# Kernel optimization log

Measured on AMD Instinct MI355X. Metric: run time of the kernel, lower is better.

The kernel has to match this reference:

```python
import jax, jax.numpy as jnp
import numpy as np
from jax import lax

V, E, HD, T = 32000, 256, 256, 4   # vocab, embed dim, lstm hidden (bidir total), tagset (BMES)
H = HD // 2                        # hidden per direction
B, S = 64, 1024


def setup_inputs() -> dict:
    key = jax.random.key(0)
    ks = jax.random.split(key, 16)
    sc = 0.1
    return {
        "sentences": jax.random.randint(ks[0], (B, S), 0, V, dtype=jnp.int32),
        "embed": jax.random.normal(ks[1], (V, E), jnp.float32) * sc,
        "w_ih_f": jax.random.normal(ks[2], (4 * H, E), jnp.float32) * sc,
        "w_hh_f": jax.random.normal(ks[3], (4 * H, H), jnp.float32) * sc,
        "b_ih_f": jax.random.normal(ks[4], (4 * H,), jnp.float32) * sc,
        "b_hh_f": jax.random.normal(ks[5], (4 * H,), jnp.float32) * sc,
        "w_ih_r": jax.random.normal(ks[6], (4 * H, E), jnp.float32) * sc,
        "w_hh_r": jax.random.normal(ks[7], (4 * H, H), jnp.float32) * sc,
        "b_ih_r": jax.random.normal(ks[8], (4 * H,), jnp.float32) * sc,
        "b_hh_r": jax.random.normal(ks[9], (4 * H,), jnp.float32) * sc,
        "w_out": jax.random.normal(ks[10], (T, HD), jnp.float32) * sc,
        "b_out": jax.random.normal(ks[11], (T,), jnp.float32) * sc,
        "start_t": jax.random.normal(ks[12], (T,), jnp.float32) * sc,
        "end_t": jax.random.normal(ks[13], (T,), jnp.float32) * sc,
        "trans": jax.random.normal(ks[14], (T, T), jnp.float32) * sc,
    }


def _lstm_pass(x, w_ih, w_hh, b_ih, b_hh):
    # x: [S, B, E]; PyTorch gate order i, f, g, o; zero initial state.
    bsz = x.shape[1]
    hdim = w_hh.shape[1]
    b = b_ih + b_hh

    def step(carry, xt):
        h, c = carry
        z = xt @ w_ih.T + h @ w_hh.T + b  # [B, 4H]
        i, f, g, o = jnp.split(z, 4, axis=-1)
        c = jax.nn.sigmoid(f) * c + jax.nn.sigmoid(i) * jnp.tanh(g)
        h = jax.nn.sigmoid(o) * jnp.tanh(c)
        return (h, c), h

    init = (jnp.zeros((bsz, hdim), x.dtype), jnp.zeros((bsz, hdim), x.dtype))
    _, hs = lax.scan(step, init, x)
    return hs  # [S, B, H]


def _emissions(sentences, embed, w_ih_f, w_hh_f, b_ih_f, b_hh_f,
               w_ih_r, w_hh_r, b_ih_r, b_hh_r, w_out, b_out):
    x = embed[sentences]                # [B, S, E]
    xs = jnp.transpose(x, (1, 0, 2))    # [S, B, E]
    hf = _lstm_pass(xs, w_ih_f, w_hh_f, b_ih_f, b_hh_f)
    hr = _lstm_pass(xs[::-1], w_ih_r, w_hh_r, b_ih_r, b_hh_r)[::-1]
    h = jnp.concatenate([hf, hr], axis=-1)        # [S, B, 2H]
    return h @ w_out.T + b_out                    # [S, B, T] emissions


def _viterbi_decode(feats, start_t, end_t, trans):
    # feats: [S, B, T] (no mask: all sequences full length, matching crf.decode on dense batch)
    score0 = start_t + feats[0]  # [B, T]

    def fwd_step(score, emit):
        nxt = score[:, :, None] + trans[None, :, :] + emit[:, None, :]  # [B, Tprev, Tcur]
        return jnp.max(nxt, axis=1), jnp.argmax(nxt, axis=1)

    final, bps = lax.scan(fwd_step, score0, feats[1:])  # bps: [S-1, B, T]
    final = final + end_t
    last = jnp.argmax(final, axis=1)  # [B]

    def back_step(tag, bp):
        prev = jnp.take_along_axis(bp, tag[:, None], axis=1)[:, 0]
        return prev, prev

    _, path_head = lax.scan(back_step, last, bps, reverse=True)  # [S-1, B], tags at t=0..S-2
    path = jnp.concatenate([path_head, last[None]], axis=0)      # [S, B]
    return jnp.transpose(path, (1, 0)).astype(jnp.int32)         # [B, S]


def reference(sentences, embed, w_ih_f, w_hh_f, b_ih_f, b_hh_f,
              w_ih_r, w_hh_r, b_ih_r, b_hh_r, w_out, b_out,
              start_t, end_t, trans):
    feats = _emissions(sentences, embed, w_ih_f, w_hh_f, b_ih_f, b_hh_f,
                       w_ih_r, w_hh_r, b_ih_r, b_hh_r, w_out, b_out)
    return _viterbi_decode(feats, start_t, end_t, trans)
```

## Files before the change

### kernel.cpp

```cpp
#include <hip/hip_runtime.h>
#include <cstdint>
#include <cstddef>

#define SLEN 1024
#define BATCH 64
#define EDIM 256
#define HDIM 128
#define GDIM 512
#define NTAG 4

typedef float f2 __attribute__((ext_vector_type(2)));
typedef float f4 __attribute__((ext_vector_type(4)));


__device__ __forceinline__ float sigm_f(float x) {
    return 1.0f / (1.0f + __expf(-x));
}
__device__ __forceinline__ float tanh_f(float x) {
    return 1.0f - 2.0f / (1.0f + __expf(2.0f * x));
}

template <int CTRL>
__device__ __forceinline__ float quad_perm(float x) {
    return __int_as_float(
        __builtin_amdgcn_mov_dpp(__float_as_int(x), CTRL, 0xF, 0xF, true));
}
#define QP_XOR1 0xB1
#define QP_XOR2 0x4E
#define QP_MIR8 0x141
#define QP_BC0  0x00
#define QP_BC1  0x55
#define QP_BC2  0xAA
#define QP_BC3  0xFF

__device__ __forceinline__ void gemm_body(
    float* smem, int mt, int cp,
    const int* __restrict__ sent, const float* __restrict__ embed,
    const float* __restrict__ w_ih_f, const float* __restrict__ w_ih_r,
    const float* __restrict__ b_ih_f, const float* __restrict__ b_hh_f,
    const float* __restrict__ b_ih_r, const float* __restrict__ b_hh_r,
    float* __restrict__ Z, int base_f, int base_r)
{
    float* As = smem;
    const int t  = threadIdx.x;
    const int tm = t >> 8;
    const int tt = t & 255;
    float* Bs = smem + 4096 + tm * 4096;

    const int nt  = cp * 2 + tm;
    const int dir = nt >> 2;
    const float* W  = dir ? w_ih_r : w_ih_f;
    const float* bi = dir ? b_ih_r : b_ih_f;
    const float* bh = dir ? b_hh_r : b_hh_f;
    const int ncol = (nt & 3) * 128;
    const int r0   = mt * 128;

    const int sra = t & 127;
    const int qa  = t >> 7;
    const int r_loc = r0 + sra;
    const int s_loc = r_loc >> 6;
    const int b_    = r_loc & 63;
    const int s_glob = (dir ? base_r : base_f) + s_loc;
    const int tok = sent[b_ * SLEN + s_glob];
    const float* arow = embed + (size_t)tok * EDIM + qa * 8;

    const int srb = tt & 127;
    const int hb  = tt >> 7;
    const float* brow = W + (size_t)(ncol + srb) * EDIM + hb * 16;

    const int tx = tt & 15, ty = tt >> 4;

    f2 acc[8][4];
    #pragma unroll
    for (int i = 0; i < 8; ++i)
        #pragma unroll
        for (int jj = 0; jj < 4; ++jj) acc[i][jj] = (f2)(0.0f);

    for (int kt = 0; kt < 8; ++kt) {
        const int k0 = kt * 32;
        __syncthreads();
        {
            float4 v0 = *(const float4*)(arow + k0);
            float4 v1 = *(const float4*)(arow + k0 + 4);
            const int kk = qa * 8;
            As[(kk + 0) * 128 + sra] = v0.x;
            As[(kk + 1) * 128 + sra] = v0.y;
            As[(kk + 2) * 128 + sra] = v0.z;
            As[(kk + 3) * 128 + sra] = v0.w;
            As[(kk + 4) * 128 + sra] = v1.x;
            As[(kk + 5) * 128 + sra] = v1.y;
            As[(kk + 6) * 128 + sra] = v1.z;
            As[(kk + 7) * 128 + sra] = v1.w;
        }
        #pragma unroll
        for (int i = 0; i < 4; ++i) {
            float4 v = *(const float4*)(brow + k0 + i * 4);
            const int kk = hb * 16 + i * 4;
            Bs[(kk + 0) * 128 + srb] = v.x;
            Bs[(kk + 1) * 128 + srb] = v.y;
            Bs[(kk + 2) * 128 + srb] = v.z;
            Bs[(kk + 3) * 128 + srb] = v.w;
        }
        __syncthreads();

        #pragma unroll 8
        for (int k = 0; k < 32; ++k) {
            const f4 a0  = *(const f4*)&As[k * 128 + ty * 4];
            const f4 a1  = *(const f4*)&As[k * 128 + 64 + ty * 4];
            const f4 bq0 = *(const f4*)&Bs[k * 128 + tx * 4];
            const f4 bq1 = *(const f4*)&Bs[k * 128 + 64 + tx * 4];
            float av[8] = {a0.x, a0.y, a0.z, a0.w, a1.x, a1.y, a1.z, a1.w};
            f2 bv[4];
            bv[0] = __builtin_shufflevector(bq0, bq0, 0, 1);
            bv[1] = __builtin_shufflevector(bq0, bq0, 2, 3);
            bv[2] = __builtin_shufflevector(bq1, bq1, 0, 1);
            bv[3] = __builtin_shufflevector(bq1, bq1, 2, 3);
            #pragma unroll
            for (int i = 0; i < 8; ++i) {
                f2 as; as.x = av[i]; as.y = av[i];
                #pragma unroll
                for (int jj = 0; jj < 4; ++jj)
                    acc[i][jj] += as * bv[jj];
            }
        }
    }

    float bias0[4], bias1[4];
    #pragma unroll
    for (int j = 0; j < 4; ++j) {
        bias0[j] = bi[ncol + tx * 4 + j] + bh[ncol + tx * 4 + j];
        bias1[j] = bi[ncol + 64 + tx * 4 + j] + bh[ncol + 64 + tx * 4 + j];
    }

    #pragma unroll
    for (int i = 0; i < 8; ++i) {
        const int row = r0 + ((i < 4) ? (ty * 4 + i) : (64 + ty * 4 + i - 4));
        float* zp = Z + (size_t)row * 1024 + dir * 512 + ncol;
        float4 o0, o1;
        o0.x = acc[i][0].x + bias0[0]; o0.y = acc[i][0].y + bias0[1];
        o0.z = acc[i][1].x + bias0[2]; o0.w = acc[i][1].y + bias0[3];
        o1.x = acc[i][2].x + bias1[0]; o1.y = acc[i][2].y + bias1[1];
        o1.z = acc[i][3].x + bias1[2]; o1.w = acc[i][3].y + bias1[3];
        *(float4*)(zp + tx * 4)      = o0;
        *(float4*)(zp + 64 + tx * 4) = o1;
    }
}

__device__ __forceinline__ void lstm_body(
    float* smem,
    const float* __restrict__ Z, const float* __restrict__ w_hh_f,
    const float* __restrict__ w_hh_r, float* __restrict__ H,
    float* __restrict__ ST, int base_f, int base_r, int L, int first)
{
    float* sh_h = smem;

    const int bid = blockIdx.x;
    const int b   = bid & 63;
    const int dir = bid >> 6;
    const int q   = threadIdx.x;
    const int p   = q & 7;
    const int Q   = q >> 3;
    const int gt  = p & 3;
    const int hi  = p >> 2;
    const int u   = Q + hi * 64;

    const float* Whh = dir ? w_hh_r : w_hh_f;

    f2 w2[8][8];
    #pragma unroll
    for (int pr = 0; pr < 8; ++pr) {
        const int uu = (pr & 4) ? (Q + 64) : Q;
        const int gg = pr & 3;
        const f2* src =
            (const f2*)(Whh + ((size_t)(gg * 128 + uu) * 128 + p * 16));
        #pragma unroll
        for (int i = 0; i < 8; ++i) w2[pr][i] = src[i];
    }

    float* stp = ST + (size_t)(dir * 64 + b) * 256;
    if (q < 128)
        sh_h[(q >> 5) * 36 + (q & 31)] = first ? 0.0f : stp[q];
    float c = first ? 0.0f : stp[128 + u];

    const ptrdiff_t zstride = dir ? -65536 : 65536;
    const float* zp0 = Z + (size_t)b * 1024 + dir * 512
                     + (dir ? (size_t)(L - 1) * 65536 : 0) + gt * 128 + u;
    const ptrdiff_t hstride = dir ? -16384 : 16384;
    float* hg = H + ((size_t)(dir ? (base_r + L - 1) : base_f) * 64 + b) * 256
              + dir * 128 + u;

    const bool k4 = (p & 4) != 0;
    const bool k2 = (p & 2) != 0;
    const bool k1 = (p & 1) != 0;
    const float gsc  = (gt == 2) ? 2.0f : 1.0f;
    const float gofs = (gt == 2) ? -1.0f : 0.0f;
    const int shr = (p >> 1) * 36 + (p & 1) * 16;
    const int shw = (u >> 5) * 36 + (u & 31);

    float zcur[4], znxt[4];
    {
        const float* zp = zp0;
        #pragma unroll
        for (int dt = 0; dt < 4; ++dt) { zcur[dt] = *zp; zp += zstride; }
    }
    __syncthreads();

    float hlast = 0.0f;

    for (int t0 = 0; t0 < L; t0 += 4) {
        const bool more = (t0 + 4 < L);
        if (more) {
            const float* zp = zp0 + (ptrdiff_t)(t0 + 4) * zstride;
            #pragma unroll
            for (int dt = 0; dt < 4; ++dt) { znxt[dt] = *zp; zp += zstride; }
        }

        #pragma unroll
        for (int dt = 0; dt < 4; ++dt) {
            const f4* hp = (const f4*)(sh_h + (dt & 1) * 160 + shr);
            f2 hv[8];
            #pragma unroll
            for (int i = 0; i < 4; ++i) {
                f4 v = hp[i];
                hv[2 * i]     = __builtin_shufflevector(v, v, 0, 1);
                hv[2 * i + 1] = __builtin_shufflevector(v, v, 2, 3);
            }
            float s[8];
            #pragma unroll
            for (int pr = 0; pr < 8; ++pr) {
                f2 a = (f2)(0.0f);
                #pragma unroll
                for (int i = 0; i < 8; ++i) a += w2[pr][i] * hv[i];
                s[pr] = a.x + a.y;
            }
            float K1[4];
            #pragma unroll
            for (int j = 0; j < 4; ++j) {
                float keep = k4 ? s[j + 4] : s[j];
                float send = k4 ? s[j] : s[j + 4];
                K1[j] = keep + quad_perm<QP_MIR8>(send);
            }
            float K2[2];
            #pragma unroll
            for (int j = 0; j < 2; ++j) {
                float keep = k2 ? K1[j + 2] : K1[j];
                float send = k2 ? K1[j] : K1[j + 2];
                K2[j] = keep + quad_perm<QP_XOR2>(send);
            }
            float keep3 = k1 ? K2[1] : K2[0];
            float send3 = k1 ? K2[0] : K2[1];
            float zv = keep3 + quad_perm<QP_XOR1>(send3) + zcur[dt];

            float sgv = sigm_f(zv * gsc);
            float act = fmaf(sgv, gsc, gofs);

            float a_i = quad_perm<QP_BC0>(act);
            float a_f = quad_perm<QP_BC1>(act);
            float a_g = quad_perm<QP_BC2>(act);
            float a_o = quad_perm<QP_BC3>(act);
            c = a_f * c + a_i * a_g;
            float h = a_o * tanh_f(c);
            hlast = h;

            if (gt == 0) {
                sh_h[((dt + 1) & 1) * 160 + shw] = h;
                *hg = h;
            }
            hg += hstride;
            __syncthreads();
        }

        if (more) {
            #pragma unroll
            for (int dt = 0; dt < 4; ++dt) zcur[dt] = znxt[dt];
        }
    }

    if (gt == 0) {
        stp[u] = hlast;
        stp[128 + u] = c;
    }
}

__global__ __launch_bounds__(512) void fused_lstm_gemm(
    const int* __restrict__ sent, const float* __restrict__ embed,
    const float* __restrict__ w_ih_f, const float* __restrict__ w_ih_r,
    const float* __restrict__ b_ih_f, const float* __restrict__ b_hh_f,
    const float* __restrict__ b_ih_r, const float* __restrict__ b_hh_r,
    float* __restrict__ Zw, int gbase_f, int gbase_r, int mtiles,
    const float* __restrict__ Zr, const float* __restrict__ w_hh_f,
    const float* __restrict__ w_hh_r, float* __restrict__ H,
    float* __restrict__ ST, int lbase_f, int lbase_r, int L, int first)
{
    __shared__ __align__(16) float smem[12288];

    if (blockIdx.x < 128) {
        lstm_body(smem, Zr, w_hh_f, w_hh_r, H, ST, lbase_f, lbase_r, L, first);
    } else {
        const int g  = blockIdx.x - 128;
        const int mt = g % mtiles;
        const int cp = g / mtiles;
        gemm_body(smem, mt, cp, sent, embed, w_ih_f, w_ih_r,
                  b_ih_f, b_hh_f, b_ih_r, b_hh_r, Zw, gbase_f, gbase_r);
    }
}

__global__ __launch_bounds__(512) void gemm_zin(
    const int* __restrict__ sent, const float* __restrict__ embed,
    const float* __restrict__ w_ih_f, const float* __restrict__ w_ih_r,
    const float* __restrict__ b_ih_f, const float* __restrict__ b_hh_f,
    const float* __restrict__ b_ih_r, const float* __restrict__ b_hh_r,
    float* __restrict__ Z, int base_f, int base_r)
{
    __shared__ __align__(16) float smem[12288];
    gemm_body(smem, blockIdx.x, blockIdx.y, sent, embed, w_ih_f, w_ih_r,
              b_ih_f, b_hh_f, b_ih_r, b_hh_r, Z, base_f, base_r);
}

__global__ __launch_bounds__(256) void emissions_k(
    const float* __restrict__ H, const float* __restrict__ w_out,
    const float* __restrict__ b_out, float* __restrict__ F)
{
    const int gid = blockIdx.x * 256 + threadIdx.x;
    const int r   = gid >> 2;
    const int tg  = gid & 3;
    const float4* h4 = (const float4*)(H + (size_t)r * 256);
    const float4* w4 = (const float4*)(w_out + (size_t)tg * 256);
    float a0 = 0.f, a1 = 0.f, a2 = 0.f, a3 = 0.f;
    #pragma unroll 8
    for (int k = 0; k < 64; ++k) {
        float4 h = h4[k], w = w4[k];
        a0 = fmaf(h.x, w.x, a0); a1 = fmaf(h.y, w.y, a1);
        a2 = fmaf(h.z, w.z, a2); a3 = fmaf(h.w, w.w, a3);
    }
    F[gid] = ((a0 + a1) + (a2 + a3)) + b_out[tg];
}

__device__ __forceinline__ unsigned compose_map(unsigned a, unsigned b) {
    unsigned r = 0;
    #pragma unroll
    for (int jj = 0; jj < 4; ++jj) {
        unsigned bj = (b >> (jj * 8)) & 3u;
        unsigned aj = (a >> (bj * 8)) & 3u;
        r |= aj << (jj * 8);
    }
    return r;
}

__global__ __launch_bounds__(64) void viterbi_k(
    const float* __restrict__ F, const float* __restrict__ start_t,
    const float* __restrict__ end_t, const float* __restrict__ trans,
    int* __restrict__ out)
{
    const int b    = blockIdx.x;
    const int lane = threadIdx.x;
    __shared__ __align__(16) float sfeat[SLEN][NTAG];
    __shared__ unsigned sbp[SLEN];

    #pragma unroll
    for (int i = 0; i < 16; ++i) {
        int s = i * 64 + lane;
        ((float4*)sfeat)[s] = *(const float4*)(F + ((size_t)s * BATCH + b) * NTAG);
    }
    __syncthreads();

    const int cur = lane & 3;
    float tr0 = trans[0 * 4 + cur], tr1 = trans[1 * 4 + cur];
    float tr2 = trans[2 * 4 + cur], tr3 = trans[3 * 4 + cur];
    float sc = start_t[cur] + sfeat[0][cur];

    for (int s = 1; s < SLEN; ++s) {
        float ft = sfeat[s][cur];
        float s0 = __shfl(sc, 0), s1 = __shfl(sc, 1);
        float s2 = __shfl(sc, 2), s3 = __shfl(sc, 3);
        float c0 = s0 + tr0, c1 = s1 + tr1, c2 = s2 + tr2, c3 = s3 + tr3;
        float best = c0; int arg = 0;
        if (c1 > best) { best = c1; arg = 1; }
        if (c2 > best) { best = c2; arg = 2; }
        if (c3 > best) { best = c3; arg = 3; }
        sc = best + ft;
        unsigned bp = (unsigned)arg;
        unsigned b0 = __shfl(bp, 0), b1 = __shfl(bp, 1);
        unsigned b2 = __shfl(bp, 2), b3 = __shfl(bp, 3);
        if (lane == 0) sbp[s] = b0 | (b1 << 8) | (b2 << 16) | (b3 << 24);
    }
    sc += end_t[cur];
    float f0 = __shfl(sc, 0), f1 = __shfl(sc, 1);
    float f2v = __shfl(sc, 2), f3 = __shfl(sc, 3);
    int last = 0; float bb = f0;
    if (f1 > bb)  { bb = f1;  last = 1; }
    if (f2v > bb) { bb = f2v; last = 2; }
    if (f3 > bb)  { bb = f3;  last = 3; }
    __syncthreads();

    unsigned m[16];
    #pragma unroll
    for (int k = 0; k < 16; ++k) {
        int s = lane * 16 + k;
        m[k] = (s >= 1) ? sbp[s] : 0x03020100u;
    }
    unsigned G = m[15];
    #pragma unroll
    for (int k = 14; k >= 0; --k) G = compose_map(m[k], G);
    unsigned R = G;
    #pragma unroll
    for (int d = 1; d < 64; d <<= 1) {
        unsigned oo = __shfl_down(R, d);
        if (lane + d < 64) R = compose_map(R, oo);
    }
    unsigned P = __shfl_down(R, 1);
    if (lane == 63) P = 0x03020100u;

    int tcur = (int)((P >> (last * 8)) & 3u);
    int* ob = out + b * SLEN + lane * 16;
    ob[15] = tcur;
    #pragma unroll
    for (int k = 15; k >= 1; --k) {
        tcur = (int)((m[k] >> (tcur * 8)) & 3u);
        ob[k - 1] = tcur;
    }
}

extern "C" void kernel_launch(void* const* d_in, const int* in_sizes, int n_in,
                              void* d_out, int out_size, void* d_ws, size_t ws_size,
                              hipStream_t stream)
{
    const int*   sent    = (const int*)d_in[0];
    const float* embed   = (const float*)d_in[1];
    const float* w_ih_f  = (const float*)d_in[2];
    const float* w_hh_f  = (const float*)d_in[3];
    const float* b_ih_f  = (const float*)d_in[4];
    const float* b_hh_f  = (const float*)d_in[5];
    const float* w_ih_r  = (const float*)d_in[6];
    const float* w_hh_r  = (const float*)d_in[7];
    const float* b_ih_r  = (const float*)d_in[8];
    const float* b_hh_r  = (const float*)d_in[9];
    const float* w_out   = (const float*)d_in[10];
    const float* b_out   = (const float*)d_in[11];
    const float* start_t = (const float*)d_in[12];
    const float* end_t   = (const float*)d_in[13];
    const float* trans   = (const float*)d_in[14];
    int* out = (int*)d_out;

    const size_t H_FLOATS  = (size_t)SLEN * BATCH * 256;
    const size_t F_FLOATS  = (size_t)SLEN * BATCH * NTAG;
    const size_t ST_FLOATS = (size_t)2 * BATCH * 256;
    const size_t FIXED = H_FLOATS + F_FLOATS + ST_FLOATS;

    int L = 0;
    for (int cand = 256; cand >= 32; cand >>= 1) {
        size_t need = ((size_t)2 * cand * BATCH * 1024 + FIXED) * sizeof(float);
        if (need <= ws_size) { L = cand; break; }
    }

    if (L > 0) {
        const int nch = SLEN / L;
        const int mtiles = (L * BATCH) / 128;
        float* Z0 = (float*)d_ws;
        float* Z1 = Z0 + (size_t)L * BATCH * 1024;
        float* H  = Z1 + (size_t)L * BATCH * 1024;
        float* F  = H + H_FLOATS;
        float* ST = F + F_FLOATS;
        float* Zb[2] = {Z0, Z1};

        gemm_zin<<<dim3(mtiles, 4), 512, 0, stream>>>(
            sent, embed, w_ih_f, w_ih_r, b_ih_f, b_hh_f, b_ih_r, b_hh_r,
            Zb[0], 0, SLEN - L);

        for (int c = 0; c < nch; ++c) {
            const int lbase_f = c * L;
            const int lbase_r = SLEN - (c + 1) * L;
            const int hasg = (c + 1 < nch);
            const int gbase_f = (c + 1) * L;
            const int gbase_r = SLEN - (c + 2) * L;
            const int grid = hasg ? (128 + mtiles * 4) : 128;
            fused_lstm_gemm<<<grid, 512, 0, stream>>>(
                sent, embed, w_ih_f, w_ih_r, b_ih_f, b_hh_f, b_ih_r, b_hh_r,
                Zb[(c + 1) & 1], hasg ? gbase_f : 0, hasg ? gbase_r : 0, mtiles,
                Zb[c & 1], w_hh_f, w_hh_r, H, ST, lbase_f, lbase_r, L,
                c == 0 ? 1 : 0);
        }

        emissions_k<<<1024, 256, 0, stream>>>(H, w_out, b_out, F);
        viterbi_k<<<64, 64, 0, stream>>>(F, start_t, end_t, trans, out);
    } else {
        int Ls = SLEN;
        while (Ls > 32) {
            size_t need = ((size_t)Ls * BATCH * 1024 + FIXED) * sizeof(float);
            if (need <= ws_size) break;
            Ls >>= 1;
        }
        const int nch = SLEN / Ls;
        const int mtiles = (Ls * BATCH) / 128;
        float* Z  = (float*)d_ws;
        float* H  = Z + (size_t)Ls * BATCH * 1024;
        float* F  = H + H_FLOATS;
        float* ST = F + F_FLOATS;

        for (int c = 0; c < nch; ++c) {
            const int base_f = c * Ls;
            const int base_r = SLEN - (c + 1) * Ls;
            gemm_zin<<<dim3(mtiles, 4), 512, 0, stream>>>(
                sent, embed, w_ih_f, w_ih_r, b_ih_f, b_hh_f, b_ih_r, b_hh_r,
                Z, base_f, base_r);
            fused_lstm_gemm<<<128, 512, 0, stream>>>(
                sent, embed, w_ih_f, w_ih_r, b_ih_f, b_hh_f, b_ih_r, b_hh_r,
                Z, 0, 0, mtiles,
                Z, w_hh_f, w_hh_r, H, ST, base_f, base_r, Ls, c == 0 ? 1 : 0);
        }
        emissions_k<<<1024, 256, 0, stream>>>(H, w_out, b_out, F);
        viterbi_k<<<64, 64, 0, stream>>>(F, start_t, end_t, trans, out);
    }
}
```

Measured before the change: 1.182 ms.

## Process two batch rows per LSTM block, streaming recurrent weights from memory

Restructures the recurrent LSTM kernel so each block advances two batch sequences at once, halving the number of LSTM blocks. Each thread now owns one hidden unit and a quarter of K for all four gates. Recurrent weights are read from global memory each step instead of being kept in registers. The intent is to amortise weight traffic across two sequences and free CUs for the overlapped input GEMM. The risk is longer per-step latency on the serial recurrence from cache-bound weight loads.

```diff
diff --git a/kernel.cpp b/kernel.cpp
--- a/kernel.cpp
+++ b/kernel.cpp
@@ -27,11 +27,12 @@
 }
 #define QP_XOR1 0xB1
 #define QP_XOR2 0x4E
-#define QP_MIR8 0x141
 #define QP_BC0  0x00
 #define QP_BC1  0x55
 #define QP_BC2  0xAA
 #define QP_BC3  0xFF
+
+#define HPAD(k) ((k) + (((k) >> 5) << 2))
 
 __device__ __forceinline__ void gemm_body(
     float* smem, int mt, int cp,
@@ -155,116 +156,141 @@
     float* sh_h = smem;
 
     const int bid = blockIdx.x;
-    const int b   = bid & 63;
-    const int dir = bid >> 6;
+    const int dir = bid >> 5;
+    const int b0  = (bid & 31) * 2;
     const int q   = threadIdx.x;
-    const int p   = q & 7;
-    const int Q   = q >> 3;
-    const int gt  = p & 3;
-    const int hi  = p >> 2;
-    const int u   = Q + hi * 64;
+    const int u   = q >> 2;
+    const int p   = q & 3;
 
     const float* Whh = dir ? w_hh_r : w_hh_f;
-
-    f2 w2[8][8];
-    #pragma unroll
-    for (int pr = 0; pr < 8; ++pr) {
-        const int uu = (pr & 4) ? (Q + 64) : Q;
-        const int gg = pr & 3;
-        const f2* src =
-            (const f2*)(Whh + ((size_t)(gg * 128 + uu) * 128 + p * 16));
-        #pragma unroll
-        for (int i = 0; i < 8; ++i) w2[pr][i] = src[i];
-    }
-
-    float* stp = ST + (size_t)(dir * 64 + b) * 256;
-    if (q < 128)
-        sh_h[(q >> 5) * 36 + (q & 31)] = first ? 0.0f : stp[q];
-    float c = first ? 0.0f : stp[128 + u];
+    const float* wbase = Whh + (size_t)u * 128 + p * 32;
+
+    float* stp0 = ST + (size_t)(dir * 64 + b0) * 256;
+
+    if (q < 256) {
+        const int bb = q >> 7, uu = q & 127;
+        sh_h[bb * 144 + HPAD(uu)] =
+            first ? 0.0f : ST[(size_t)(dir * 64 + b0 + bb) * 256 + uu];
+    }
+    float c0 = first ? 0.0f : stp0[128 + u];
+    float c1 = first ? 0.0f : stp0[256 + 128 + u];
 
     const ptrdiff_t zstride = dir ? -65536 : 65536;
-    const float* zp0 = Z + (size_t)b * 1024 + dir * 512
-                     + (dir ? (size_t)(L - 1) * 65536 : 0) + gt * 128 + u;
+    const float* zp0 = Z + (size_t)b0 * 1024 + dir * 512 + p * 128 + u
+                     + (dir ? (size_t)(L - 1) * 65536 : 0);
     const ptrdiff_t hstride = dir ? -16384 : 16384;
-    float* hg = H + ((size_t)(dir ? (base_r + L - 1) : base_f) * 64 + b) * 256
+    float* hg = H + ((size_t)(dir ? (base_r + L - 1) : base_f) * 64 + b0) * 256
               + dir * 128 + u;
 
-    const bool k4 = (p & 4) != 0;
     const bool k2 = (p & 2) != 0;
     const bool k1 = (p & 1) != 0;
-    const float gsc  = (gt == 2) ? 2.0f : 1.0f;
-    const float gofs = (gt == 2) ? -1.0f : 0.0f;
-    const int shr = (p >> 1) * 36 + (p & 1) * 16;
-    const int shw = (u >> 5) * 36 + (u & 31);
-
-    float zcur[4], znxt[4];
+    const float gsc  = (p == 2) ? 2.0f : 1.0f;
+    const float gofs = (p == 2) ? -1.0f : 0.0f;
+    const int rbase = 36 * p;
+
+    float zc[4][2], zn[4][2];
     {
         const float* zp = zp0;
         #pragma unroll
-        for (int dt = 0; dt < 4; ++dt) { zcur[dt] = *zp; zp += zstride; }
+        for (int dt = 0; dt < 4; ++dt) {
+            zc[dt][0] = zp[0]; zc[dt][1] = zp[1024]; zp += zstride;
+        }
     }
     __syncthreads();
 
-    float hlast = 0.0f;
+    float h0l = 0.0f, h1l = 0.0f;
 
     for (int t0 = 0; t0 < L; t0 += 4) {
         const bool more = (t0 + 4 < L);
         if (more) {
             const float* zp = zp0 + (ptrdiff_t)(t0 + 4) * zstride;
             #pragma unroll
-            for (int dt = 0; dt < 4; ++dt) { znxt[dt] = *zp; zp += zstride; }
+            for (int dt = 0; dt < 4; ++dt) {
+                zn[dt][0] = zp[0]; zn[dt][1] = zp[1024]; zp += zstride;
+            }
         }
 
         #pragma unroll
         for (int dt = 0; dt < 4; ++dt) {
-            const f4* hp = (const f4*)(sh_h + (dt & 1) * 160 + shr);
-            f2 hv[8];
-            #pragma unroll
-            for (int i = 0; i < 4; ++i) {
-                f4 v = hp[i];
-                hv[2 * i]     = __builtin_shufflevector(v, v, 0, 1);
-                hv[2 * i + 1] = __builtin_shufflevector(v, v, 2, 3);
-            }
-            float s[8];
-            #pragma unroll
-            for (int pr = 0; pr < 8; ++pr) {
-                f2 a = (f2)(0.0f);
+            float* shb = sh_h + ((t0 + dt) & 1) * 288;
+            f2 acc[4][2];
+            #pragma unroll
+            for (int g = 0; g < 4; ++g) {
+                acc[g][0] = (f2)(0.0f); acc[g][1] = (f2)(0.0f);
+            }
+
+            #pragma unroll
+            for (int kh = 0; kh < 2; ++kh) {
+                const f4* h0p = (const f4*)(shb + rbase + kh * 16);
+                const f4* h1p = (const f4*)(shb + 144 + rbase + kh * 16);
+                f2 ha[8], hb2[8];
                 #pragma unroll
-                for (int i = 0; i < 8; ++i) a += w2[pr][i] * hv[i];
-                s[pr] = a.x + a.y;
-            }
-            float K1[4];
-            #pragma unroll
-            for (int j = 0; j < 4; ++j) {
-                float keep = k4 ? s[j + 4] : s[j];
-                float send = k4 ? s[j] : s[j + 4];
-                K1[j] = keep + quad_perm<QP_MIR8>(send);
-            }
-            float K2[2];
+                for (int i = 0; i < 4; ++i) {
+                    f4 va = h0p[i], vb = h1p[i];
+                    ha[2*i]    = __builtin_shufflevector(va, va, 0, 1);
+                    ha[2*i+1]  = __builtin_shufflevector(va, va, 2, 3);
+                    hb2[2*i]   = __builtin_shufflevector(vb, vb, 0, 1);
+                    hb2[2*i+1] = __builtin_shufflevector(vb, vb, 2, 3);
+                }
+                #pragma unroll
+                for (int g = 0; g < 4; ++g) {
+                    const f4* wp = (const f4*)(wbase + (size_t)g * 16384
+                                               + kh * 16);
+                    #pragma unroll
+                    for (int i = 0; i < 4; ++i) {
+                        f4 wv = wp[i];
+                        f2 w0 = __builtin_shufflevector(wv, wv, 0, 1);
+                        f2 w1 = __builtin_shufflevector(wv, wv, 2, 3);
+                        acc[g][0] += w0 * ha[2*i];
+                        acc[g][0] += w1 * ha[2*i+1];
+                        acc[g][1] += w0 * hb2[2*i];
+                        acc[g][1] += w1 * hb2[2*i+1];
+                    }
+                }
+            }
+
+            float s[4][2];
+            #pragma unroll
+            for (int g = 0; g < 4; ++g) {
+                s[g][0] = acc[g][0].x + acc[g][0].y;
+                s[g][1] = acc[g][1].x + acc[g][1].y;
+            }
+            float A0[2], A1[2];
             #pragma unroll
             for (int j = 0; j < 2; ++j) {
-                float keep = k2 ? K1[j + 2] : K1[j];
-                float send = k2 ? K1[j] : K1[j + 2];
-                K2[j] = keep + quad_perm<QP_XOR2>(send);
-            }
-            float keep3 = k1 ? K2[1] : K2[0];
-            float send3 = k1 ? K2[0] : K2[1];
-            float zv = keep3 + quad_perm<QP_XOR1>(send3) + zcur[dt];
-
-            float sgv = sigm_f(zv * gsc);
-            float act = fmaf(sgv, gsc, gofs);
-
-            float a_i = quad_perm<QP_BC0>(act);
-            float a_f = quad_perm<QP_BC1>(act);
-            float a_g = quad_perm<QP_BC2>(act);
-            float a_o = quad_perm<QP_BC3>(act);
-            c = a_f * c + a_i * a_g;
-            float h = a_o * tanh_f(c);
-            hlast = h;
-
-            if (gt == 0) {
-                sh_h[((dt + 1) & 1) * 160 + shw] = h;
-                *hg = h;
+                float ke0 = k2 ? s[j+2][0] : s[j][0];
+                float se0 = k2 ? s[j][0] : s[j+2][0];
+                A0[j] = ke0 + quad_perm<QP_XOR2>(se0);
+                float ke1 = k2 ? s[j+2][1] : s[j][1];
+                float se1 = k2 ? s[j][1] : s[j+2][1];
+                A1[j] = ke1 + quad_perm<QP_XOR2>(se1);
+            }
+            float ka = k1 ? A0[1] : A0[0];
+            float sa = k1 ? A0[0] : A0[1];
+            float z0 = ka + quad_perm<QP_XOR1>(sa) + zc[dt][0];
+            float kb = k1 ? A1[1] : A1[0];
+            float sb = k1 ? A1[0] : A1[1];
+            float z1 = kb + quad_perm<QP_XOR1>(sb) + zc[dt][1];
+
+            float a0 = fmaf(sigm_f(z0 * gsc), gsc, gofs);
+            float a1 = fmaf(sigm_f(z1 * gsc), gsc, gofs);
+
+            float i0 = quad_perm<QP_BC0>(a0), f0v = quad_perm<QP_BC1>(a0);
+            float g0v = quad_perm<QP_BC2>(a0), o0 = quad_perm<QP_BC3>(a0);
+            c0 = f0v * c0 + i0 * g0v;
+            float h0 = o0 * tanh_f(c0);
+            float i1 = quad_perm<QP_BC0>(a1), f1v = quad_perm<QP_BC1>(a1);
+            float g1v = quad_perm<QP_BC2>(a1), o1 = quad_perm<QP_BC3>(a1);
+            c1 = f1v * c1 + i1 * g1v;
+            float h1 = o1 * tanh_f(c1);
+            h0l = h0; h1l = h1;
+
+            if (p == 0) {
+                float* shn = sh_h + ((t0 + dt + 1) & 1) * 288;
+                shn[HPAD(u)] = h0;
+                shn[144 + HPAD(u)] = h1;
+                hg[0]   = h0;
+                hg[256] = h1;
             }
             hg += hstride;
             __syncthreads();
@@ -272,13 +298,15 @@
 
         if (more) {
             #pragma unroll
-            for (int dt = 0; dt < 4; ++dt) zcur[dt] = znxt[dt];
-        }
-    }
-
-    if (gt == 0) {
-        stp[u] = hlast;
-        stp[128 + u] = c;
+            for (int dt = 0; dt < 4; ++dt) {
+                zc[dt][0] = zn[dt][0]; zc[dt][1] = zn[dt][1];
+            }
+        }
+    }
+
+    if (p == 0) {
+        stp0[u] = h0l;        stp0[128 + u] = c0;
+        stp0[256 + u] = h1l;  stp0[256 + 128 + u] = c1;
     }
 }
 
@@ -294,10 +322,10 @@
 {
     __shared__ __align__(16) float smem[12288];
 
-    if (blockIdx.x < 128) {
+    if (blockIdx.x < 64) {
         lstm_body(smem, Zr, w_hh_f, w_hh_r, H, ST, lbase_f, lbase_r, L, first);
     } else {
-        const int g  = blockIdx.x - 128;
+        const int g  = blockIdx.x - 64;
         const int mt = g % mtiles;
         const int cp = g / mtiles;
         gemm_body(smem, mt, cp, sent, embed, w_ih_f, w_ih_r,
@@ -473,7 +501,7 @@
             const int hasg = (c + 1 < nch);
             const int gbase_f = (c + 1) * L;
             const int gbase_r = SLEN - (c + 2) * L;
-            const int grid = hasg ? (128 + mtiles * 4) : 128;
+            const int grid = hasg ? (64 + mtiles * 4) : 64;
             fused_lstm_gemm<<<grid, 512, 0, stream>>>(
                 sent, embed, w_ih_f, w_ih_r, b_ih_f, b_hh_f, b_ih_r, b_hh_r,
                 Zb[(c + 1) & 1], hasg ? gbase_f : 0, hasg ? gbase_r : 0, mtiles,
@@ -503,7 +531,7 @@
             gemm_zin<<<dim3(mtiles, 4), 512, 0, stream>>>(
                 sent, embed, w_ih_f, w_ih_r, b_ih_f, b_hh_f, b_ih_r, b_hh_r,
                 Z, base_f, base_r);
-            fused_lstm_gemm<<<128, 512, 0, stream>>>(
+            fused_lstm_gemm<<<64, 512, 0, stream>>>(
                 sent, embed, w_ih_f, w_ih_r, b_ih_f, b_hh_f, b_ih_r, b_hh_r,
                 Z, 0, 0, mtiles,
                 Z, w_hh_f, w_hh_r, H, ST, base_f, base_r, Ls, c == 0 ? 1 : 0);
```

Result: slower. 1.551 ms (+31.2%).
